# Performance work log

Hardware: AMD Instinct MI355X
Metric: run time of the kernel (lower is better)

The kernel has to match this reference:

```python
import jax, jax.numpy as jnp
import numpy as np

N_VEH, N_PED = 16, 16
DV, DP = 40, 24            # vehicle / pedestrian slot obs dims
N = N_VEH + N_PED          # 32 agents
E, H = 128, 4              # embed_dim, num_heads
DH = E // H                # head_dim = 32
B = 4096
OBS = N_VEH * DV + N_PED * DP + N  # 1056


def setup_inputs() -> dict:
    key = jax.random.key(0)
    ks = jax.random.split(key, 12)
    s = lambda fan_in: 1.0 / np.sqrt(fan_in)
    inp = {
        "global_obs": jax.random.uniform(ks[0], (B, OBS), dtype=jnp.float32),
        # per-type projectors (stored as (in, out) so x @ W + b)
        "Wv": jax.random.uniform(ks[1], (DV, E), jnp.float32, -s(DV), s(DV)),
        "bv": jax.random.uniform(ks[2], (E,), jnp.float32, -s(DV), s(DV)),
        "Wp": jax.random.uniform(ks[3], (DP, E), jnp.float32, -s(DP), s(DP)),
        "bp": jax.random.uniform(ks[4], (E,), jnp.float32, -s(DP), s(DP)),
        # GAT layer 0 / 1: w (E, H*DH), a_src / a_dst (H, DH)
        "w0": jax.random.normal(ks[5], (E, H * DH), jnp.float32) * s(E),
        "asrc0": jax.random.normal(ks[6], (H, DH), jnp.float32) * s(DH),
        "adst0": jax.random.normal(ks[7], (H, DH), jnp.float32) * s(DH),
        "w1": jax.random.normal(ks[8], (E, H * DH), jnp.float32) * s(E),
        "asrc1": jax.random.normal(ks[9], (H, DH), jnp.float32) * s(DH),
        "adst1": jax.random.normal(ks[10], (H, DH), jnp.float32) * s(DH),
    }
    return inp


def _gat(x, alive, w, a_src, a_dst):
    # x: (B,N,E), alive: (B,N) in {0,1}
    b, n, _ = x.shape
    h = (x @ w).reshape(b, n, H, DH)                       # (B,N,H,DH)
    alpha_src = jnp.einsum("bnhd,hd->bnh", h, a_src)       # (B,N,H)
    alpha_dst = jnp.einsum("bnhd,hd->bnh", h, a_dst)
    e = alpha_src[:, :, None, :] + alpha_dst[:, None, :, :]  # (B,Ni,Nj,H)
    e = jnp.where(e > 0, e, 0.2 * e)                       # LeakyReLU(0.2)
    key_mask = alive[:, None, :, None] >= 0.5              # mask over j
    e = jnp.where(key_mask, e, -jnp.inf)
    attn = jax.nn.softmax(e, axis=2)                       # softmax over keys j
    attn = jnp.nan_to_num(attn)
    out = jnp.einsum("bijh,bjhd->bihd", attn, h)           # weighted aggregate
    return out.reshape(b, n, H * DH)                       # concat heads


def reference(global_obs, Wv, bv, Wp, bp, w0, asrc0, adst0, w1, asrc1, adst1):
    b = global_obs.shape[0]
    veh = global_obs[:, : N_VEH * DV].reshape(b, N_VEH, DV)
    ped = global_obs[:, N_VEH * DV : N_VEH * DV + N_PED * DP].reshape(b, N_PED, DP)
    alive_raw = global_obs[:, -N:]
    tokens = jnp.concatenate([veh @ Wv + bv, ped @ Wp + bp], axis=1)  # (B,N,E)
    alive = (alive_raw >= 0.5).astype(jnp.float32)
    all_dead = jnp.sum(alive, axis=1, keepdims=True) < 0.5
    alive = jnp.where(all_dead, jnp.ones_like(alive), alive)
    x = tokens
    for (w, a_s, a_d) in ((w0, asrc0, adst0), (w1, asrc1, adst1)):
        x = jax.nn.elu(_gat(x, alive, w, a_s, a_d))
    aw = alive[:, :, None]
    pooled = jnp.sum(x * aw, axis=1) / jnp.clip(jnp.sum(aw, axis=1), 1.0)
    return pooled
```

## Files before the change

kernel.cpp:

```cpp
#include <hip/hip_runtime.h>


#define NTOK 32
#define EMB  128
#define OBSL 1056
#define XSTR 136
#define HSTR 40
#define TILE 5120

typedef __attribute__((ext_vector_type(8))) short  short8;
typedef __attribute__((ext_vector_type(4))) float  floatx4;
typedef __attribute__((ext_vector_type(2))) unsigned uint2v;

__device__ __forceinline__ short f2bf(float f) {
  union { float f; unsigned u; } v; v.f = f;
  unsigned r = (v.u + 0x7fffu + ((v.u >> 16) & 1u)) >> 16;
  return (short)(unsigned short)r;
}
__device__ __forceinline__ unsigned pk2(float a, float b) {
  unsigned r; asm("v_cvt_pk_bf16_f32 %0, %1, %2" : "=v"(r) : "v"(a), "v"(b)); return r;
}
__device__ __forceinline__ float exp2_hw(float x) {
#if __has_builtin(__builtin_amdgcn_exp2f)
  return __builtin_amdgcn_exp2f(x);
#else
  return exp2f(x);
#endif
}
__device__ __forceinline__ float rcp_hw(float x) {
#if __has_builtin(__builtin_amdgcn_rcpf)
  return __builtin_amdgcn_rcpf(x);
#else
  return 1.0f / x;
#endif
}
__device__ __forceinline__ float elu1(float v) { return v > 0.f ? v : __expf(v) - 1.f; }
__device__ __forceinline__ floatx4 mfma16(short8 a, short8 b, floatx4 c) {
  return __builtin_amdgcn_mfma_f32_16x16x32_bf16(a, b, c, 0, 0, 0);
}

__global__ void prep_weights(const float* __restrict__ Wv, const float* __restrict__ Wp,
                             const float* __restrict__ w0, const float* __restrict__ w1,
                             short* __restrict__ ws) {
  int idx = blockIdx.x * 256 + threadIdx.x;
  if (idx < 8192) {
    int e = idx >> 6, k = idx & 63;
    float v = (k < 40) ? Wv[(size_t)k * EMB + e] : Wp[(size_t)(k - 40) * EMB + e];
    ws[idx] = f2bf(v);
  } else if (idx < 24576) {
    int t = idx - 8192; int e = t >> 7, k = t & 127;
    ws[idx] = f2bf(w0[(size_t)k * EMB + e]);
  } else {
    int t = idx - 24576; int e = t >> 7, k = t & 127;
    ws[idx] = f2bf(w1[(size_t)k * EMB + e]);
  }
}

__global__ __launch_bounds__(256, 8) void gnn_fused(
    const float* __restrict__ obs,
    const float* __restrict__ bv, const float* __restrict__ bp,
    const float* __restrict__ as0, const float* __restrict__ ad0,
    const float* __restrict__ as1, const float* __restrict__ ad1,
    const short* __restrict__ wsb,
    float* __restrict__ out)
{
  __shared__ __align__(16) short s_t[2][TILE];

  const int tid  = threadIdx.x;
  const int lane = tid & 63;
  const int wv   = tid >> 6;
  const int item = wv >> 1;
  const int hw   = wv & 1;
  const int col  = lane & 15;
  const int quad = lane >> 4;
  const int b    = blockIdx.x * 2 + item;

  const float* orow = obs + (size_t)b * OBSL;
  short* xbase = s_t[item];
  short* hbase = &s_t[item][hw * 2560];
  const short8  z8 = {0,0,0,0,0,0,0,0};
  const floatx4 fz = {0.f,0.f,0.f,0.f};

  float flag; float invc;
  {
    float araw = (lane < NTOK) ? orow[1024 + lane] : 0.f;
    bool alv = (lane < NTOK) && (araw >= 0.5f);
    unsigned long long m = __ballot(alv);
    int cnt = __popcll(m);
    flag = alv ? 1.f : 0.f;
    if (cnt == 0) { flag = (lane < NTOK) ? 1.f : 0.f; cnt = NTOK; }
    invc = 1.f / (float)cnt;
  }
  const float alvI0 = __shfl(flag, col);
  const float alvI1 = __shfl(flag, 16 + col);

  #pragma unroll
  for (int it = 0; it < 2; ++it) {
    int c = (hw * 2 + it) * 64 + lane;
    *(short8*)&xbase[(c >> 3) * XSTR + (c & 7) * 8] = z8;
  }
  __syncthreads();
  #pragma unroll
  for (int it = 0; it < 2; ++it) {
    int i4 = (hw * 2 + it) * 64 + lane;
    float4 v = *(const float4*)&orow[i4 * 4];
    int r, k;
    if (i4 < 160) { r = (i4 * 205) >> 11;  k = (i4 - r * 10) * 4; }
    else { int t2 = i4 - 160; int q6 = (t2 * 171) >> 10; r = 16 + q6; k = 40 + (t2 - q6 * 6) * 4; }
    uint2v u; u.x = pk2(v.x, v.y); u.y = pk2(v.z, v.w);
    *(uint2v*)&xbase[r * XSTR + k] = u;
  }
  __syncthreads();

  {
    short8 Bxin[2][2];
    #pragma unroll
    for (int nt = 0; nt < 2; ++nt)
      #pragma unroll
      for (int kt = 0; kt < 2; ++kt)
        Bxin[nt][kt] = *(const short8*)&xbase[(nt * 16 + col) * XSTR + kt * 32 + quad * 8];
    __syncthreads();
    const short* embT = wsb;
    #pragma unroll
    for (int mi = 0; mi < 4; ++mi) {
      const int mtE = hw * 4 + mi;
      short8 A0 = *(const short8*)&embT[(mtE * 16 + col) * 64 + quad * 8];
      short8 A1 = *(const short8*)&embT[(mtE * 16 + col) * 64 + 32 + quad * 8];
      float4 bv4 = *(const float4*)&bv[mtE * 16 + quad * 4];
      float4 bp4 = *(const float4*)&bp[mtE * 16 + quad * 4];
      #pragma unroll
      for (int nt = 0; nt < 2; ++nt) {
        floatx4 acc = fz;
        acc = mfma16(A0, Bxin[nt][0], acc);
        acc = mfma16(A1, Bxin[nt][1], acc);
        float4 bb = nt ? bp4 : bv4;
        uint2v u; u.x = pk2(acc[0] + bb.x, acc[1] + bb.y); u.y = pk2(acc[2] + bb.z, acc[3] + bb.w);
        *(uint2v*)&xbase[(nt * 16 + col) * XSTR + mtE * 16 + quad * 4] = u;
      }
    }
  }

  for (int L = 0; L < 2; ++L) {
    const short* wT  = wsb + 8192 + L * 16384;
    const float* gas = L ? as1 : as0;
    const float* gad = L ? ad1 : ad0;

    __syncthreads();

    short8 Bx[4][2];
    #pragma unroll
    for (int kt = 0; kt < 4; ++kt)
      #pragma unroll
      for (int nt = 0; nt < 2; ++nt)
        Bx[kt][nt] = *(const short8*)&xbase[(nt * 16 + col) * XSTR + kt * 32 + quad * 8];
    __syncthreads();

    float psrc[2][2], pdst[2][2];
    #pragma unroll
    for (int hl = 0; hl < 2; ++hl) { psrc[hl][0]=0.f; psrc[hl][1]=0.f; pdst[hl][0]=0.f; pdst[hl][1]=0.f; }
    #pragma unroll
    for (int g = 0; g < 2; ++g) {
      floatx4 acc[2][2];
      #pragma unroll
      for (int mi = 0; mi < 2; ++mi) { acc[mi][0] = fz; acc[mi][1] = fz; }
      #pragma unroll
      for (int mi = 0; mi < 2; ++mi) {
        const int mt = hw * 4 + g * 2 + mi;
        const short* wrow = &wT[(mt * 16 + col) * 128 + quad * 8];
        short8 A0 = *(const short8*)&wrow[0];
        short8 A1 = *(const short8*)&wrow[32];
        short8 A2 = *(const short8*)&wrow[64];
        short8 A3 = *(const short8*)&wrow[96];
        #pragma unroll
        for (int nt = 0; nt < 2; ++nt) {
          acc[mi][nt] = mfma16(A0, Bx[0][nt], acc[mi][nt]);
          acc[mi][nt] = mfma16(A1, Bx[1][nt], acc[mi][nt]);
          acc[mi][nt] = mfma16(A2, Bx[2][nt], acc[mi][nt]);
          acc[mi][nt] = mfma16(A3, Bx[3][nt], acc[mi][nt]);
        }
      }
      #pragma unroll
      for (int mi = 0; mi < 2; ++mi) {
        const int mt = hw * 4 + g * 2 + mi;
        float4 cs = *(const float4*)&gas[mt * 16 + quad * 4];
        float4 cd = *(const float4*)&gad[mt * 16 + quad * 4];
        const int rowloc = (g * 2 + mi) * 16 + quad * 4;
        #pragma unroll
        for (int nt = 0; nt < 2; ++nt) {
          floatx4 a = acc[mi][nt];
          psrc[g][nt] += a[0]*cs.x + a[1]*cs.y + a[2]*cs.z + a[3]*cs.w;
          pdst[g][nt] += a[0]*cd.x + a[1]*cd.y + a[2]*cd.z + a[3]*cd.w;
          unsigned u01 = pk2(a[0], a[1]);
          unsigned u23 = pk2(a[2], a[3]);
          unsigned short* hrow = (unsigned short*)&hbase[rowloc * HSTR + nt * 16 + col];
          hrow[0]        = (unsigned short)u01;
          hrow[HSTR]     = (unsigned short)(u01 >> 16);
          hrow[2 * HSTR] = (unsigned short)u23;
          hrow[3 * HSTR] = (unsigned short)(u23 >> 16);
        }
      }
    }

    #pragma unroll
    for (int hl = 0; hl < 2; ++hl)
      #pragma unroll
      for (int nt = 0; nt < 2; ++nt) {
        float vs = psrc[hl][nt]; vs += __shfl_xor(vs, 16); vs += __shfl_xor(vs, 32);
        psrc[hl][nt] = vs * 1.44269504088896340736f;
        float vd = pdst[hl][nt]; vd += __shfl_xor(vd, 16); vd += __shfl_xor(vd, 32);
        pdst[hl][nt] = vd * 1.44269504088896340736f;
      }

    float alv8[8];
    #pragma unroll
    for (int jj = 0; jj < 8; ++jj) alv8[jj] = __shfl(flag, quad * 8 + jj);

    short8 pf[2][2];
    #pragma unroll
    for (int hl = 0; hl < 2; ++hl) {
      float vsel = (quad >> 1) ? pdst[hl][1] : pdst[hl][0];
      float ad8[8];
      #pragma unroll
      for (int jj = 0; jj < 8; ++jj) {
        float v = __shfl(vsel, ((quad >> 1) << 5) + ((quad & 1) << 3) + jj);
        ad8[jj] = (alv8[jj] >= 0.5f) ? v : -1e30f;
      }
      #pragma unroll
      for (int ii = 0; ii < 2; ++ii) {
        float ai = psrc[hl][ii];
        float ev[8]; float sum = 0.f;
        #pragma unroll
        for (int jj = 0; jj < 8; ++jj) {
          float e = ai + ad8[jj];
          e = fmaxf(e, 0.2f * e);
          float p = exp2_hw(e);
          ev[jj] = p; sum += p;
        }
        sum += __shfl_xor(sum, 16);
        sum += __shfl_xor(sum, 32);
        float inv = rcp_hw(sum);
        union { unsigned u4[4]; short8 s; } pu;
        #pragma unroll
        for (int p2 = 0; p2 < 4; ++p2) pu.u4[p2] = pk2(ev[2*p2] * inv, ev[2*p2+1] * inv);
        pf[hl][ii] = pu.s;
      }
    }

    short8 Ah[2][2];
    #pragma unroll
    for (int hl = 0; hl < 2; ++hl)
      #pragma unroll
      for (int mt2 = 0; mt2 < 2; ++mt2)
        Ah[hl][mt2] = *(const short8*)&hbase[(hl * 32 + mt2 * 16 + col) * HSTR + quad * 8];
    if (L == 0) __syncthreads();

    #pragma unroll
    for (int hl = 0; hl < 2; ++hl)
      #pragma unroll
      for (int mt2 = 0; mt2 < 2; ++mt2) {
        floatx4 po[2];
        #pragma unroll
        for (int nt = 0; nt < 2; ++nt) {
          po[nt] = mfma16(Ah[hl][mt2], pf[hl][nt], fz);
        }
        const int ecol = hw * 64 + hl * 32 + mt2 * 16 + quad * 4;
        if (L == 0) {
          #pragma unroll
          for (int nt = 0; nt < 2; ++nt) {
            uint2v u;
            u.x = pk2(elu1(po[nt][0]), elu1(po[nt][1]));
            u.y = pk2(elu1(po[nt][2]), elu1(po[nt][3]));
            *(uint2v*)&xbase[(nt * 16 + col) * XSTR + ecol] = u;
          }
        } else {
          #pragma unroll
          for (int r = 0; r < 4; ++r) {
            float s = elu1(po[0][r]) * alvI0 + elu1(po[1][r]) * alvI1;
            s += __shfl_xor(s, 1); s += __shfl_xor(s, 2);
            s += __shfl_xor(s, 4); s += __shfl_xor(s, 8);
            if (col == 0) out[(size_t)b * EMB + ecol + r] = s * invc;
          }
        }
      }
  }
}

extern "C" void kernel_launch(void* const* d_in, const int* in_sizes, int n_in,
                              void* d_out, int out_size, void* d_ws, size_t ws_size,
                              hipStream_t stream) {
  const float* obs = (const float*)d_in[0];
  const float* Wv  = (const float*)d_in[1];
  const float* bv  = (const float*)d_in[2];
  const float* Wp  = (const float*)d_in[3];
  const float* bp  = (const float*)d_in[4];
  const float* w0  = (const float*)d_in[5];
  const float* as0 = (const float*)d_in[6];
  const float* ad0 = (const float*)d_in[7];
  const float* w1  = (const float*)d_in[8];
  const float* as1 = (const float*)d_in[9];
  const float* ad1 = (const float*)d_in[10];
  float* out = (float*)d_out;
  short* wsb = (short*)d_ws;

  int Bn = in_sizes[0] / OBSL;
  prep_weights<<<160, 256, 0, stream>>>(Wv, Wp, w0, w1, wsb);
  gnn_fused<<<Bn / 2, 256, 0, stream>>>(obs, bv, bp, as0, ad0, as1, ad1, wsb, out);
}
```

Measured before the change: 160.6 us.

## Interleave GAT projection MFMAs over k-tiles and relax launch bounds

Restructures the per-layer projection GEMM so x operand fragments are loaded one k-tile at a time and all four m-tiles accumulate together, instead of preloading all eight B fragments and then processing m-tiles in two groups. The attention-logit reductions now run before the barrier that guards the shared buffer, and the bf16 stores of h move after that barrier. Launch bounds drop from 8 to 6 waves per SIMD, giving the compiler more registers for the eight live accumulators. The intent is fewer register spills and better MFMA/LDS interleaving, at the cost of lower possible occupancy.

```diff
diff --git a/kernel.cpp b/kernel.cpp
--- a/kernel.cpp
+++ b/kernel.cpp
@@ -56,7 +56,7 @@
   }
 }
 
-__global__ __launch_bounds__(256, 8) void gnn_fused(
+__global__ __launch_bounds__(256, 6) void gnn_fused(
     const float* __restrict__ obs,
     const float* __restrict__ bv, const float* __restrict__ bp,
     const float* __restrict__ as0, const float* __restrict__ ad0,
@@ -147,57 +147,53 @@
 
     __syncthreads();
 
-    short8 Bx[4][2];
-    #pragma unroll
-    for (int kt = 0; kt < 4; ++kt)
-      #pragma unroll
-      for (int nt = 0; nt < 2; ++nt)
-        Bx[kt][nt] = *(const short8*)&xbase[(nt * 16 + col) * XSTR + kt * 32 + quad * 8];
+    floatx4 acc[4][2];
+    #pragma unroll
+    for (int mi = 0; mi < 4; ++mi) { acc[mi][0] = fz; acc[mi][1] = fz; }
+    #pragma unroll
+    for (int kt = 0; kt < 4; ++kt) {
+      short8 B0 = *(const short8*)&xbase[(col) * XSTR + kt * 32 + quad * 8];
+      short8 B1 = *(const short8*)&xbase[(16 + col) * XSTR + kt * 32 + quad * 8];
+      #pragma unroll
+      for (int mi = 0; mi < 4; ++mi) {
+        const int mt = hw * 4 + mi;
+        short8 A = *(const short8*)&wT[(mt * 16 + col) * 128 + kt * 32 + quad * 8];
+        acc[mi][0] = mfma16(A, B0, acc[mi][0]);
+        acc[mi][1] = mfma16(A, B1, acc[mi][1]);
+      }
+    }
+
+    float psrc[2][2], pdst[2][2];
+    #pragma unroll
+    for (int hl = 0; hl < 2; ++hl) { psrc[hl][0]=0.f; psrc[hl][1]=0.f; pdst[hl][0]=0.f; pdst[hl][1]=0.f; }
+    #pragma unroll
+    for (int mi = 0; mi < 4; ++mi) {
+      const int mt = hw * 4 + mi;
+      const int hl = mi >> 1;
+      float4 cs = *(const float4*)&gas[mt * 16 + quad * 4];
+      float4 cd = *(const float4*)&gad[mt * 16 + quad * 4];
+      #pragma unroll
+      for (int nt = 0; nt < 2; ++nt) {
+        floatx4 a = acc[mi][nt];
+        psrc[hl][nt] += a[0]*cs.x + a[1]*cs.y + a[2]*cs.z + a[3]*cs.w;
+        pdst[hl][nt] += a[0]*cd.x + a[1]*cd.y + a[2]*cd.z + a[3]*cd.w;
+      }
+    }
     __syncthreads();
 
-    float psrc[2][2], pdst[2][2];
-    #pragma unroll
-    for (int hl = 0; hl < 2; ++hl) { psrc[hl][0]=0.f; psrc[hl][1]=0.f; pdst[hl][0]=0.f; pdst[hl][1]=0.f; }
-    #pragma unroll
-    for (int g = 0; g < 2; ++g) {
-      floatx4 acc[2][2];
-      #pragma unroll
-      for (int mi = 0; mi < 2; ++mi) { acc[mi][0] = fz; acc[mi][1] = fz; }
-      #pragma unroll
-      for (int mi = 0; mi < 2; ++mi) {
-        const int mt = hw * 4 + g * 2 + mi;
-        const short* wrow = &wT[(mt * 16 + col) * 128 + quad * 8];
-        short8 A0 = *(const short8*)&wrow[0];
-        short8 A1 = *(const short8*)&wrow[32];
-        short8 A2 = *(const short8*)&wrow[64];
-        short8 A3 = *(const short8*)&wrow[96];
-        #pragma unroll
-        for (int nt = 0; nt < 2; ++nt) {
-          acc[mi][nt] = mfma16(A0, Bx[0][nt], acc[mi][nt]);
-          acc[mi][nt] = mfma16(A1, Bx[1][nt], acc[mi][nt]);
-          acc[mi][nt] = mfma16(A2, Bx[2][nt], acc[mi][nt]);
-          acc[mi][nt] = mfma16(A3, Bx[3][nt], acc[mi][nt]);
-        }
-      }
-      #pragma unroll
-      for (int mi = 0; mi < 2; ++mi) {
-        const int mt = hw * 4 + g * 2 + mi;
-        float4 cs = *(const float4*)&gas[mt * 16 + quad * 4];
-        float4 cd = *(const float4*)&gad[mt * 16 + quad * 4];
-        const int rowloc = (g * 2 + mi) * 16 + quad * 4;
-        #pragma unroll
-        for (int nt = 0; nt < 2; ++nt) {
-          floatx4 a = acc[mi][nt];
-          psrc[g][nt] += a[0]*cs.x + a[1]*cs.y + a[2]*cs.z + a[3]*cs.w;
-          pdst[g][nt] += a[0]*cd.x + a[1]*cd.y + a[2]*cd.z + a[3]*cd.w;
-          unsigned u01 = pk2(a[0], a[1]);
-          unsigned u23 = pk2(a[2], a[3]);
-          unsigned short* hrow = (unsigned short*)&hbase[rowloc * HSTR + nt * 16 + col];
-          hrow[0]        = (unsigned short)u01;
-          hrow[HSTR]     = (unsigned short)(u01 >> 16);
-          hrow[2 * HSTR] = (unsigned short)u23;
-          hrow[3 * HSTR] = (unsigned short)(u23 >> 16);
-        }
+    #pragma unroll
+    for (int mi = 0; mi < 4; ++mi) {
+      const int rowloc = mi * 16 + quad * 4;
+      #pragma unroll
+      for (int nt = 0; nt < 2; ++nt) {
+        floatx4 a = acc[mi][nt];
+        unsigned u01 = pk2(a[0], a[1]);
+        unsigned u23 = pk2(a[2], a[3]);
+        unsigned short* hrow = (unsigned short*)&hbase[rowloc * HSTR + nt * 16 + col];
+        hrow[0]        = (unsigned short)u01;
+        hrow[HSTR]     = (unsigned short)(u01 >> 16);
+        hrow[2 * HSTR] = (unsigned short)u23;
+        hrow[3 * HSTR] = (unsigned short)(u23 >> 16);
       }
     }
 
```

Result: faster. 143.4 us (-10.7%).
